# Kernel optimization log

Hardware: AMD Instinct MI355X
Metric: run time of the kernel (lower is better)

The kernel has to match this reference:

```python
import jax, jax.numpy as jnp
import numpy as np

B, S, C, H = 1, 512, 384, 12
SQK, SV, PQK, PV = 16, 16, 4, 8
SCALAR_SCALE = SQK ** -0.5
NEG = jnp.float32(-10000.0)


def _random_rotations(key, shape):
    # Gram-Schmidt on random normals -> proper rotation matrices (rows orthonormal)
    m = jax.random.normal(key, shape + (3, 3), jnp.float32)
    e0 = m[..., 0, :]
    e0 = e0 / jnp.linalg.norm(e0, axis=-1, keepdims=True)
    e1 = m[..., 1, :] - jnp.sum(e0 * m[..., 1, :], axis=-1, keepdims=True) * e0
    e1 = e1 / jnp.linalg.norm(e1, axis=-1, keepdims=True)
    e2 = jnp.cross(e0, e1)
    return jnp.stack([e0, e1, e2], axis=-2)  # [..., 3, 3]


def setup_inputs() -> dict:
    key = jax.random.key(0)
    ks = jax.random.split(key, 24)
    rn = lambda k, shp, s=1.0: jax.random.normal(k, shp, jnp.float32) * s
    w = 0.02  # weight init scale
    inp = {
        'single_repr': rn(ks[0], (B, S, C)),
        'rotations': _random_rotations(ks[1], (B, S)),
        'translations': rn(ks[2], (B, S, 3), 10.0),
        'Wq_s': rn(ks[3], (C, H * SQK), w), 'bq_s': rn(ks[4], (H * SQK,), w),
        'Wk_s': rn(ks[5], (C, H * SQK), w), 'bk_s': rn(ks[6], (H * SQK,), w),
        'Wv_s': rn(ks[7], (C, H * SV), w), 'bv_s': rn(ks[8], (H * SV,), w),
        'Wq_p': rn(ks[9], (C, H * PQK * 3), w), 'bq_p': rn(ks[10], (H * PQK * 3,), w),
        'Wk_p': rn(ks[11], (C, H * PQK * 3), w), 'bk_p': rn(ks[12], (H * PQK * 3,), w),
        'Wv_p': rn(ks[13], (C, H * PV * 3), w), 'bv_p': rn(ks[14], (H * PV * 3,), w),
        'point_weights': rn(ks[15], (H, PQK), 0.5),
        'Wo': rn(ks[16], (H * (SV + PV * 4), C), w), 'bo': rn(ks[17], (C,), w),
        'valid_mask': jax.random.randint(ks[18], (B, S), 0, 2).astype(bool),
    }
    return inp


def _ipa(single_repr, rotations, translations,
         Wq_s, bq_s, Wk_s, bk_s, Wv_s, bv_s,
         Wq_p, bq_p, Wk_p, bk_p, Wv_p, bv_p,
         point_weights, Wo, bo, valid_mask):
    b, s, _ = single_repr.shape
    qs = (single_repr @ Wq_s + bq_s).reshape(b, s, H, SQK)
    ks = (single_repr @ Wk_s + bk_s).reshape(b, s, H, SQK)
    vs = (single_repr @ Wv_s + bv_s).reshape(b, s, H, SV)
    qp = (single_repr @ Wq_p + bq_p).reshape(b, s, H, PQK, 3)
    kp = (single_repr @ Wk_p + bk_p).reshape(b, s, H, PQK, 3)
    vp = (single_repr @ Wv_p + bv_p).reshape(b, s, H, PV, 3)
    t = translations[:, :, None, None, :]
    # local -> global: R @ p + t
    qpg = jnp.einsum('bsij,bshpj->bshpi', rotations, qp) + t
    kpg = jnp.einsum('bsij,bshpj->bshpi', rotations, kp) + t
    vpg = jnp.einsum('bsij,bshpj->bshpi', rotations, vp) + t
    scalar_logits = jnp.einsum('bihd,bjhd->bhij', qs, ks) * SCALAR_SCALE
    # pairwise point distances: [b, i, j, h, p]
    delta = qpg[:, :, None] - kpg[:, None]  # [b, i, j, h, p, 3]
    dist2 = jnp.sum(delta * delta, axis=-1)
    sp_w = jax.nn.softplus(point_weights)  # [H, PQK]
    point_logits = -0.5 * jnp.einsum('bijhp,hp->bhij', dist2, sp_w)
    logits = scalar_logits + point_logits
    key_mask = valid_mask[:, None, None, :]
    logits = jnp.where(key_mask, logits, NEG)
    attn = jax.nn.softmax(logits, axis=-1)
    attn = attn * valid_mask[:, None, :, None].astype(attn.dtype)
    scalar_out = jnp.einsum('bhij,bjhd->bihd', attn, vs).reshape(b, s, H * SV)
    pog = jnp.einsum('bhij,bjhpd->bihpd', attn, vpg)  # [b, s, H, PV, 3]
    # global -> local: R^T (x - t)
    pol = jnp.einsum('bsji,bshpj->bshpi', rotations, pog - t)
    point_norm = jnp.sqrt(jnp.sum(pol * pol, axis=-1))  # [b, s, H, PV]
    combined = jnp.concatenate([
        scalar_out,
        pol.reshape(b, s, H * PV * 3),
        point_norm.reshape(b, s, H * PV),
    ], axis=-1)
    update = combined @ Wo + bo
    return update * valid_mask[..., None].astype(update.dtype)


def reference(single_repr, rotations, translations,
              Wq_s, bq_s, Wk_s, bk_s, Wv_s, bv_s,
              Wq_p, bq_p, Wk_p, bk_p, Wv_p, bv_p,
              point_weights, Wo, bo, valid_mask):
    return _ipa(single_repr, rotations, translations,
                Wq_s, bq_s, Wk_s, bk_s, Wv_s, bv_s,
                Wq_p, bq_p, Wk_p, bk_p, Wv_p, bv_p,
                point_weights, Wo, bo, valid_mask)
```

## Files before the change

kernel.cpp:

```cpp
#include <hip/hip_runtime.h>
#include <math.h>

#define S 512
#define C 384
#define H 12
#define SCALAR_SCALE 0.25f
#define NEG_LOGIT (-10000.0f)

#define XCOLS 1152
#define DQK 28
#define DV 40

__global__ __launch_bounds__(256)
void wcat_kernel(const float* __restrict__ Wq_s, const float* __restrict__ bq_s,
                 const float* __restrict__ Wk_s, const float* __restrict__ bk_s,
                 const float* __restrict__ Wv_s, const float* __restrict__ bv_s,
                 const float* __restrict__ Wq_p, const float* __restrict__ bq_p,
                 const float* __restrict__ Wk_p, const float* __restrict__ bk_p,
                 const float* __restrict__ Wv_p, const float* __restrict__ bv_p,
                 float* __restrict__ Wcat, float* __restrict__ bcat)
{
    const int NW4 = 384 * (XCOLS / 4);
    int t = blockIdx.x * 256 + threadIdx.x;
    if (t < NW4) {
        int k = t / (XCOLS / 4);
        int col = (t - k * (XCOLS / 4)) * 4;
        const float* src;
        if      (col < 192) src = Wq_s + k * 192 + col;
        else if (col < 384) src = Wk_s + k * 192 + (col - 192);
        else if (col < 576) src = Wv_s + k * 192 + (col - 384);
        else if (col < 720) src = Wq_p + k * 144 + (col - 576);
        else if (col < 864) src = Wk_p + k * 144 + (col - 720);
        else                src = Wv_p + k * 288 + (col - 864);
        ((float4*)Wcat)[t] = *(const float4*)src;
    } else if (t < NW4 + XCOLS / 4) {
        int col = (t - NW4) * 4;
        const float* src;
        if      (col < 192) src = bq_s + col;
        else if (col < 384) src = bk_s + (col - 192);
        else if (col < 576) src = bv_s + (col - 384);
        else if (col < 720) src = bq_p + (col - 576);
        else if (col < 864) src = bk_p + (col - 720);
        else                src = bv_p + (col - 864);
        ((float4*)bcat)[t - NW4] = *(const float4*)src;
    }
}

__global__ __launch_bounds__(256)
void gemm64(const float* __restrict__ A, int lda,
            const float* __restrict__ B, int ldb,
            const float* __restrict__ bias,
            float* __restrict__ Cc, int ldc, int K)
{
    __shared__ float As[16][65];
    __shared__ float Bs[16][65];
    const int tid = threadIdx.x;
    const int m0 = blockIdx.y * 64;
    const int n0 = blockIdx.x * 64;
    const int ty = tid >> 4;
    const int tx = tid & 15;

    float acc[4][4] = {};

    for (int k0 = 0; k0 < K; k0 += 16) {
        {
            int r = tid >> 2;
            int c = (tid & 3) * 4;
            const float4 v = *(const float4*)(A + (size_t)(m0 + r) * lda + k0 + c);
            As[c + 0][r] = v.x; As[c + 1][r] = v.y;
            As[c + 2][r] = v.z; As[c + 3][r] = v.w;
        }
        {
            int r = tid >> 4;
            int c = (tid & 15) * 4;
            const float4 v = *(const float4*)(B + (size_t)(k0 + r) * ldb + n0 + c);
            Bs[r][c + 0] = v.x; Bs[r][c + 1] = v.y;
            Bs[r][c + 2] = v.z; Bs[r][c + 3] = v.w;
        }
        __syncthreads();
        #pragma unroll
        for (int k = 0; k < 16; ++k) {
            float a[4], b[4];
            #pragma unroll
            for (int i = 0; i < 4; ++i) a[i] = As[k][ty * 4 + i];
            #pragma unroll
            for (int j = 0; j < 4; ++j) b[j] = Bs[k][tx * 4 + j];
            #pragma unroll
            for (int i = 0; i < 4; ++i)
                #pragma unroll
                for (int j = 0; j < 4; ++j)
                    acc[i][j] += a[i] * b[j];
        }
        __syncthreads();
    }

    #pragma unroll
    for (int i = 0; i < 4; ++i) {
        int m = m0 + ty * 4 + i;
        #pragma unroll
        for (int j = 0; j < 4; ++j) {
            int n = n0 + tx * 4 + j;
            Cc[(size_t)m * ldc + n] = acc[i][j] + bias[n];
        }
    }
}

__global__ __launch_bounds__(256)
void gemm_out(const float* __restrict__ A, int lda,
              const float* __restrict__ B, int ldb,
              const float* __restrict__ bias,
              float* __restrict__ Cc, int ldc, int K,
              const int* __restrict__ rowMask)
{
    __shared__ float As[16][33];
    __shared__ float Bs[16][33];
    const int tid = threadIdx.x;
    const int m0 = blockIdx.y * 32;
    const int n0 = blockIdx.x * 32;
    const int ty = tid >> 4;
    const int tx = tid & 15;

    float acc[2][2] = {};

    for (int k0 = 0; k0 < K; k0 += 16) {
        {
            int r = tid >> 3;
            int c = (tid & 7) * 2;
            const float2 v = *(const float2*)(A + (size_t)(m0 + r) * lda + k0 + c);
            As[c + 0][r] = v.x; As[c + 1][r] = v.y;
        }
        {
            int r = tid >> 4;
            int c = (tid & 15) * 2;
            const float2 v = *(const float2*)(B + (size_t)(k0 + r) * ldb + n0 + c);
            Bs[r][c + 0] = v.x; Bs[r][c + 1] = v.y;
        }
        __syncthreads();
        #pragma unroll
        for (int k = 0; k < 16; ++k) {
            float a0 = As[k][ty * 2], a1 = As[k][ty * 2 + 1];
            float b0 = Bs[k][tx * 2], b1 = Bs[k][tx * 2 + 1];
            acc[0][0] += a0 * b0; acc[0][1] += a0 * b1;
            acc[1][0] += a1 * b0; acc[1][1] += a1 * b1;
        }
        __syncthreads();
    }

    #pragma unroll
    for (int i = 0; i < 2; ++i) {
        int m = m0 + ty * 2 + i;
        float msk = rowMask[m] ? 1.0f : 0.0f;
        #pragma unroll
        for (int j = 0; j < 2; ++j) {
            int n = n0 + tx * 2 + j;
            Cc[(size_t)m * ldc + n] = (acc[i][j] + bias[n]) * msk;
        }
    }
}

__global__ __launch_bounds__(256)
void ipa_points(const float* __restrict__ X,
                const float* __restrict__ rot,
                const float* __restrict__ trans,
                const float* __restrict__ pw,
                float4* __restrict__ Q4, float4* __restrict__ K4,
                float4* __restrict__ V4, float* __restrict__ kb)
{
    int idx = blockIdx.x * 256 + threadIdx.x;
    int h = idx >> 9;
    int s = idx & 511;

    float R[9], t[3];
    #pragma unroll
    for (int i = 0; i < 9; ++i) R[i] = rot[s * 9 + i];
    #pragma unroll
    for (int i = 0; i < 3; ++i) t[i] = trans[s * 3 + i];

    float spw[4];
    #pragma unroll
    for (int p = 0; p < 4; ++p)
        spw[p] = log1pf(__expf(pw[h * 4 + p]));

    const float4* xr4 = (const float4*)(X + (size_t)s * XCOLS);

    float qv[DQK], kv[DQK], vv[DV];
    #pragma unroll
    for (int g = 0; g < 4; ++g) {
        float4 a = xr4[h * 4 + g];
        qv[g * 4 + 0] = a.x * SCALAR_SCALE; qv[g * 4 + 1] = a.y * SCALAR_SCALE;
        qv[g * 4 + 2] = a.z * SCALAR_SCALE; qv[g * 4 + 3] = a.w * SCALAR_SCALE;
        float4 b = xr4[48 + h * 4 + g];
        kv[g * 4 + 0] = b.x; kv[g * 4 + 1] = b.y; kv[g * 4 + 2] = b.z; kv[g * 4 + 3] = b.w;
        float4 c = xr4[96 + h * 4 + g];
        vv[g * 4 + 0] = c.x; vv[g * 4 + 1] = c.y; vv[g * 4 + 2] = c.z; vv[g * 4 + 3] = c.w;
    }
    float qp[12], kp[12], vp[24];
    #pragma unroll
    for (int g = 0; g < 3; ++g) {
        float4 a = xr4[144 + h * 3 + g];
        qp[g * 4 + 0] = a.x; qp[g * 4 + 1] = a.y; qp[g * 4 + 2] = a.z; qp[g * 4 + 3] = a.w;
        float4 b = xr4[180 + h * 3 + g];
        kp[g * 4 + 0] = b.x; kp[g * 4 + 1] = b.y; kp[g * 4 + 2] = b.z; kp[g * 4 + 3] = b.w;
    }
    #pragma unroll
    for (int g = 0; g < 6; ++g) {
        float4 a = xr4[216 + h * 6 + g];
        vp[g * 4 + 0] = a.x; vp[g * 4 + 1] = a.y; vp[g * 4 + 2] = a.z; vp[g * 4 + 3] = a.w;
    }

    float knorm = 0.0f;
    #pragma unroll
    for (int p = 0; p < 4; ++p) {
        #pragma unroll
        for (int i = 0; i < 3; ++i) {
            float qg = R[i * 3] * qp[p * 3] + R[i * 3 + 1] * qp[p * 3 + 1] + R[i * 3 + 2] * qp[p * 3 + 2] + t[i];
            float kg = R[i * 3] * kp[p * 3] + R[i * 3 + 1] * kp[p * 3 + 1] + R[i * 3 + 2] * kp[p * 3 + 2] + t[i];
            qv[16 + p * 3 + i] = spw[p] * qg;
            kv[16 + p * 3 + i] = kg;
            knorm += spw[p] * kg * kg;
        }
    }
    kb[(size_t)h * S + s] = -0.5f * knorm;

    #pragma unroll
    for (int p = 0; p < 8; ++p) {
        #pragma unroll
        for (int i = 0; i < 3; ++i)
            vv[16 + p * 3 + i] = R[i * 3] * vp[p * 3] + R[i * 3 + 1] * vp[p * 3 + 1] + R[i * 3 + 2] * vp[p * 3 + 2] + t[i];
    }

    #pragma unroll
    for (int g = 0; g < 7; ++g)
        Q4[((size_t)h * 7 + g) * S + s] = make_float4(qv[g * 4], qv[g * 4 + 1], qv[g * 4 + 2], qv[g * 4 + 3]);
    #pragma unroll
    for (int g = 0; g < 7; ++g)
        K4[((size_t)h * 7 + g) * S + s] = make_float4(kv[g * 4], kv[g * 4 + 1], kv[g * 4 + 2], kv[g * 4 + 3]);
    #pragma unroll
    for (int g = 0; g < 10; ++g)
        V4[((size_t)h * 10 + g) * S + s] = make_float4(vv[g * 4], vv[g * 4 + 1], vv[g * 4 + 2], vv[g * 4 + 3]);
}

__global__ __launch_bounds__(256)
void ipa_attn(const float4* __restrict__ Q4, const float4* __restrict__ K4,
              const float4* __restrict__ V4, const float* __restrict__ kb,
              const int* __restrict__ valid,
              const float* __restrict__ rot, const float* __restrict__ trans,
              float* __restrict__ combined)
{
    __shared__ float4 sh[4][10];
    const int h = blockIdx.x;
    const int wave = threadIdx.x >> 6;
    const int lane = threadIdx.x & 63;
    const int i = blockIdx.y * 4 + wave;

    float q[DQK];
    #pragma unroll
    for (int g = 0; g < 7; ++g) {
        float4 v = Q4[((size_t)h * 7 + g) * S + i];
        q[g * 4] = v.x; q[g * 4 + 1] = v.y; q[g * 4 + 2] = v.z; q[g * 4 + 3] = v.w;
    }

    const float* kbh = kb + (size_t)h * S;

    float logit[8];
    float mx = -3.0e38f;
    #pragma unroll
    for (int t = 0; t < 8; ++t) {
        int j = t * 64 + lane;
        float dot = kbh[j];
        #pragma unroll
        for (int g = 0; g < 7; ++g) {
            float4 k = K4[((size_t)h * 7 + g) * S + j];
            dot += q[g * 4] * k.x + q[g * 4 + 1] * k.y + q[g * 4 + 2] * k.z + q[g * 4 + 3] * k.w;
        }
        logit[t] = valid[j] ? dot : NEG_LOGIT;
        mx = fmaxf(mx, logit[t]);
    }
    #pragma unroll
    for (int off = 32; off >= 1; off >>= 1)
        mx = fmaxf(mx, __shfl_xor(mx, off, 64));

    float sum = 0.0f;
    #pragma unroll
    for (int t = 0; t < 8; ++t) {
        logit[t] = __expf(logit[t] - mx);
        sum += logit[t];
    }
    #pragma unroll
    for (int off = 32; off >= 1; off >>= 1)
        sum += __shfl_xor(sum, off, 64);
    const float inv = 1.0f / sum;

    float4 acc[10];
    #pragma unroll
    for (int g = 0; g < 10; ++g) acc[g] = make_float4(0.f, 0.f, 0.f, 0.f);
    #pragma unroll
    for (int t = 0; t < 8; ++t) {
        int j = t * 64 + lane;
        float p = logit[t];
        #pragma unroll
        for (int g = 0; g < 10; ++g) {
            float4 v = V4[((size_t)h * 10 + g) * S + j];
            acc[g].x += p * v.x; acc[g].y += p * v.y;
            acc[g].z += p * v.z; acc[g].w += p * v.w;
        }
    }
    #pragma unroll
    for (int g = 0; g < 10; ++g) {
        #pragma unroll
        for (int off = 32; off >= 1; off >>= 1) {
            acc[g].x += __shfl_xor(acc[g].x, off, 64);
            acc[g].y += __shfl_xor(acc[g].y, off, 64);
            acc[g].z += __shfl_xor(acc[g].z, off, 64);
            acc[g].w += __shfl_xor(acc[g].w, off, 64);
        }
    }

    if (lane == 0) {
        #pragma unroll
        for (int g = 0; g < 10; ++g) sh[wave][g] = acc[g];
    }
    const float* shf = (const float*)sh[wave];

    float* crow = combined + (size_t)i * 576;
    if (lane < 16)
        crow[h * 16 + lane] = shf[lane] * inv;

    if (lane < 8) {
        float R[9], t_[3];
        #pragma unroll
        for (int a = 0; a < 9; ++a) R[a] = rot[i * 9 + a];
        #pragma unroll
        for (int a = 0; a < 3; ++a) t_[a] = trans[i * 3 + a];
        int p = lane;
        float d0 = shf[16 + p * 3 + 0] * inv - t_[0];
        float d1 = shf[16 + p * 3 + 1] * inv - t_[1];
        float d2 = shf[16 + p * 3 + 2] * inv - t_[2];
        float pol0 = R[0] * d0 + R[3] * d1 + R[6] * d2;
        float pol1 = R[1] * d0 + R[4] * d1 + R[7] * d2;
        float pol2 = R[2] * d0 + R[5] * d1 + R[8] * d2;
        crow[192 + h * 24 + p * 3 + 0] = pol0;
        crow[192 + h * 24 + p * 3 + 1] = pol1;
        crow[192 + h * 24 + p * 3 + 2] = pol2;
        crow[480 + h * 8 + p] = sqrtf(pol0 * pol0 + pol1 * pol1 + pol2 * pol2);
    }
}

extern "C" void kernel_launch(void* const* d_in, const int* in_sizes, int n_in,
                              void* d_out, int out_size, void* d_ws, size_t ws_size,
                              hipStream_t stream)
{
    const float* single = (const float*)d_in[0];
    const float* rot    = (const float*)d_in[1];
    const float* trans  = (const float*)d_in[2];
    const float* Wq_s   = (const float*)d_in[3];
    const float* bq_s   = (const float*)d_in[4];
    const float* Wk_s   = (const float*)d_in[5];
    const float* bk_s   = (const float*)d_in[6];
    const float* Wv_s   = (const float*)d_in[7];
    const float* bv_s   = (const float*)d_in[8];
    const float* Wq_p   = (const float*)d_in[9];
    const float* bq_p   = (const float*)d_in[10];
    const float* Wk_p   = (const float*)d_in[11];
    const float* bk_p   = (const float*)d_in[12];
    const float* Wv_p   = (const float*)d_in[13];
    const float* bv_p   = (const float*)d_in[14];
    const float* pw     = (const float*)d_in[15];
    const float* Wo     = (const float*)d_in[16];
    const float* bo     = (const float*)d_in[17];
    const int*   valid  = (const int*)d_in[18];

    float* ws = (float*)d_ws;
    float* Wcat     = ws;
    float* bcat     = Wcat + (size_t)384 * XCOLS;
    float* X        = bcat + XCOLS;
    float* Q4f      = X + (size_t)S * XCOLS;
    float* K4f      = Q4f + (size_t)H * 7 * S * 4;
    float* V4f      = K4f + (size_t)H * 7 * S * 4;
    float* kbb      = V4f + (size_t)H * 10 * S * 4;
    float* combined = kbb + (size_t)H * S;

    dim3 blk(256);

    wcat_kernel<<<dim3((384 * (XCOLS / 4) + XCOLS / 4 + 255) / 256), blk, 0, stream>>>(
        Wq_s, bq_s, Wk_s, bk_s, Wv_s, bv_s, Wq_p, bq_p, Wk_p, bk_p, Wv_p, bv_p, Wcat, bcat);

    gemm64<<<dim3(XCOLS / 64, S / 64), blk, 0, stream>>>(single, C, Wcat, XCOLS, bcat, X, XCOLS, C);

    ipa_points<<<dim3(S * H / 256), blk, 0, stream>>>(X, rot, trans, pw,
                                                      (float4*)Q4f, (float4*)K4f, (float4*)V4f, kbb);

    ipa_attn<<<dim3(H, S / 4), blk, 0, stream>>>((const float4*)Q4f, (const float4*)K4f,
                                                 (const float4*)V4f, kbb, valid, rot, trans, combined);

    gemm_out<<<dim3(C / 32, S / 32), blk, 0, stream>>>(combined, 576, Wo, C, bo, (float*)d_out, C, 576, valid);
}
```

Before: 192.5 us.

## Fuse weight concat into projection GEMM and stage K/V tiles in LDS with online softmax

Drops the separate weight/bias concatenation kernel: the projection GEMM now chooses its source weight matrix per thread column and writes float4 outputs with the bias added. The attention kernel now double-buffers each 64-key chunk of K and V in shared memory, shared by the four query waves of a block, and uses an online softmax with a running max and rescaling. This is meant to cut redundant global K/V reads and one launch. In exchange it adds two barriers per chunk, an extra exp per step and more LDS use per block.

```diff
diff --git a/kernel.cpp b/kernel.cpp
--- a/kernel.cpp
+++ b/kernel.cpp
@@ -12,45 +12,14 @@
 #define DV 40
 
 __global__ __launch_bounds__(256)
-void wcat_kernel(const float* __restrict__ Wq_s, const float* __restrict__ bq_s,
-                 const float* __restrict__ Wk_s, const float* __restrict__ bk_s,
-                 const float* __restrict__ Wv_s, const float* __restrict__ bv_s,
-                 const float* __restrict__ Wq_p, const float* __restrict__ bq_p,
-                 const float* __restrict__ Wk_p, const float* __restrict__ bk_p,
-                 const float* __restrict__ Wv_p, const float* __restrict__ bv_p,
-                 float* __restrict__ Wcat, float* __restrict__ bcat)
-{
-    const int NW4 = 384 * (XCOLS / 4);
-    int t = blockIdx.x * 256 + threadIdx.x;
-    if (t < NW4) {
-        int k = t / (XCOLS / 4);
-        int col = (t - k * (XCOLS / 4)) * 4;
-        const float* src;
-        if      (col < 192) src = Wq_s + k * 192 + col;
-        else if (col < 384) src = Wk_s + k * 192 + (col - 192);
-        else if (col < 576) src = Wv_s + k * 192 + (col - 384);
-        else if (col < 720) src = Wq_p + k * 144 + (col - 576);
-        else if (col < 864) src = Wk_p + k * 144 + (col - 720);
-        else                src = Wv_p + k * 288 + (col - 864);
-        ((float4*)Wcat)[t] = *(const float4*)src;
-    } else if (t < NW4 + XCOLS / 4) {
-        int col = (t - NW4) * 4;
-        const float* src;
-        if      (col < 192) src = bq_s + col;
-        else if (col < 384) src = bk_s + (col - 192);
-        else if (col < 576) src = bv_s + (col - 384);
-        else if (col < 720) src = bq_p + (col - 576);
-        else if (col < 864) src = bk_p + (col - 720);
-        else                src = bv_p + (col - 864);
-        ((float4*)bcat)[t - NW4] = *(const float4*)src;
-    }
-}
-
-__global__ __launch_bounds__(256)
-void gemm64(const float* __restrict__ A, int lda,
-            const float* __restrict__ B, int ldb,
-            const float* __restrict__ bias,
-            float* __restrict__ Cc, int ldc, int K)
+void gemm_proj(const float* __restrict__ A,
+               const float* __restrict__ Wq_s, const float* __restrict__ bq_s,
+               const float* __restrict__ Wk_s, const float* __restrict__ bk_s,
+               const float* __restrict__ Wv_s, const float* __restrict__ bv_s,
+               const float* __restrict__ Wq_p, const float* __restrict__ bq_p,
+               const float* __restrict__ Wk_p, const float* __restrict__ bk_p,
+               const float* __restrict__ Wv_p, const float* __restrict__ bv_p,
+               float* __restrict__ X)
 {
     __shared__ float As[16][65];
     __shared__ float Bs[16][65];
@@ -60,20 +29,29 @@
     const int ty = tid >> 4;
     const int tx = tid & 15;
 
+    const int n = n0 + tx * 4;
+    const float* bsrc; const float* bbias; int ldbs, ncol;
+    if      (n < 192) { bsrc = Wq_s; bbias = bq_s; ldbs = 192; ncol = n; }
+    else if (n < 384) { bsrc = Wk_s; bbias = bk_s; ldbs = 192; ncol = n - 192; }
+    else if (n < 576) { bsrc = Wv_s; bbias = bv_s; ldbs = 192; ncol = n - 384; }
+    else if (n < 720) { bsrc = Wq_p; bbias = bq_p; ldbs = 144; ncol = n - 576; }
+    else if (n < 864) { bsrc = Wk_p; bbias = bk_p; ldbs = 144; ncol = n - 720; }
+    else              { bsrc = Wv_p; bbias = bv_p; ldbs = 288; ncol = n - 864; }
+
     float acc[4][4] = {};
 
-    for (int k0 = 0; k0 < K; k0 += 16) {
+    for (int k0 = 0; k0 < C; k0 += 16) {
         {
             int r = tid >> 2;
             int c = (tid & 3) * 4;
-            const float4 v = *(const float4*)(A + (size_t)(m0 + r) * lda + k0 + c);
+            const float4 v = *(const float4*)(A + (size_t)(m0 + r) * C + k0 + c);
             As[c + 0][r] = v.x; As[c + 1][r] = v.y;
             As[c + 2][r] = v.z; As[c + 3][r] = v.w;
         }
         {
             int r = tid >> 4;
-            int c = (tid & 15) * 4;
-            const float4 v = *(const float4*)(B + (size_t)(k0 + r) * ldb + n0 + c);
+            const float4 v = *(const float4*)(bsrc + (size_t)(k0 + r) * ldbs + ncol);
+            int c = tx * 4;
             Bs[r][c + 0] = v.x; Bs[r][c + 1] = v.y;
             Bs[r][c + 2] = v.z; Bs[r][c + 3] = v.w;
         }
@@ -94,14 +72,13 @@
         __syncthreads();
     }
 
+    const float4 bb = *(const float4*)(bbias + ncol);
     #pragma unroll
     for (int i = 0; i < 4; ++i) {
         int m = m0 + ty * 4 + i;
-        #pragma unroll
-        for (int j = 0; j < 4; ++j) {
-            int n = n0 + tx * 4 + j;
-            Cc[(size_t)m * ldc + n] = acc[i][j] + bias[n];
-        }
+        float4 o = make_float4(acc[i][0] + bb.x, acc[i][1] + bb.y,
+                               acc[i][2] + bb.z, acc[i][3] + bb.w);
+        *(float4*)(X + (size_t)m * XCOLS + n) = o;
     }
 }
 
@@ -247,10 +224,13 @@
               const float* __restrict__ rot, const float* __restrict__ trans,
               float* __restrict__ combined)
 {
+    __shared__ float4 Kl[2][448];
+    __shared__ float4 Vl[2][640];
     __shared__ float4 sh[4][10];
     const int h = blockIdx.x;
-    const int wave = threadIdx.x >> 6;
-    const int lane = threadIdx.x & 63;
+    const int tid = threadIdx.x;
+    const int wave = tid >> 6;
+    const int lane = tid & 63;
     const int i = blockIdx.y * 4 + wave;
 
     float q[DQK];
@@ -259,52 +239,80 @@
         float4 v = Q4[((size_t)h * 7 + g) * S + i];
         q[g * 4] = v.x; q[g * 4 + 1] = v.y; q[g * 4 + 2] = v.z; q[g * 4 + 3] = v.w;
     }
-
-    const float* kbh = kb + (size_t)h * S;
-
-    float logit[8];
-    float mx = -3.0e38f;
+    float kbv[8]; int vld[8];
     #pragma unroll
     for (int t = 0; t < 8; ++t) {
-        int j = t * 64 + lane;
-        float dot = kbh[j];
+        kbv[t] = kb[(size_t)h * S + t * 64 + lane];
+        vld[t] = valid[t * 64 + lane];
+    }
+
+    Kl[0][tid] = K4[((size_t)h * 7 + (tid >> 6)) * S + (tid & 63)];
+    if (tid < 192)
+        Kl[0][tid + 256] = K4[((size_t)h * 7 + ((tid + 256) >> 6)) * S + ((tid + 256) & 63)];
+    Vl[0][tid] = V4[((size_t)h * 10 + (tid >> 6)) * S + (tid & 63)];
+    Vl[0][tid + 256] = V4[((size_t)h * 10 + ((tid + 256) >> 6)) * S + ((tid + 256) & 63)];
+    if (tid < 128)
+        Vl[0][tid + 512] = V4[((size_t)h * 10 + ((tid + 512) >> 6)) * S + ((tid + 512) & 63)];
+
+    float4 acc[10];
+    #pragma unroll
+    for (int g = 0; g < 10; ++g) acc[g] = make_float4(0.f, 0.f, 0.f, 0.f);
+    float m = -3.0e38f, sum = 0.0f;
+    float4 rk0, rk1, rv0, rv1, rv2;
+
+    #pragma unroll
+    for (int t = 0; t < 8; ++t) {
+        const int b = t & 1, nb = b ^ 1;
+        if (t < 7) {
+            const int t0 = (t + 1) * 64;
+            rk0 = K4[((size_t)h * 7 + (tid >> 6)) * S + t0 + (tid & 63)];
+            if (tid < 192)
+                rk1 = K4[((size_t)h * 7 + ((tid + 256) >> 6)) * S + t0 + ((tid + 256) & 63)];
+            rv0 = V4[((size_t)h * 10 + (tid >> 6)) * S + t0 + (tid & 63)];
+            rv1 = V4[((size_t)h * 10 + ((tid + 256) >> 6)) * S + t0 + ((tid + 256) & 63)];
+            if (tid < 128)
+                rv2 = V4[((size_t)h * 10 + ((tid + 512) >> 6)) * S + t0 + ((tid + 512) & 63)];
+        }
+        __syncthreads();
+
+        float dot = kbv[t];
         #pragma unroll
         for (int g = 0; g < 7; ++g) {
-            float4 k = K4[((size_t)h * 7 + g) * S + j];
+            float4 k = Kl[b][g * 64 + lane];
             dot += q[g * 4] * k.x + q[g * 4 + 1] * k.y + q[g * 4 + 2] * k.z + q[g * 4 + 3] * k.w;
         }
-        logit[t] = valid[j] ? dot : NEG_LOGIT;
-        mx = fmaxf(mx, logit[t]);
-    }
-    #pragma unroll
-    for (int off = 32; off >= 1; off >>= 1)
-        mx = fmaxf(mx, __shfl_xor(mx, off, 64));
-
-    float sum = 0.0f;
-    #pragma unroll
-    for (int t = 0; t < 8; ++t) {
-        logit[t] = __expf(logit[t] - mx);
-        sum += logit[t];
-    }
+        float lg = vld[t] ? dot : NEG_LOGIT;
+        float lm = lg;
+        #pragma unroll
+        for (int off = 32; off >= 1; off >>= 1)
+            lm = fmaxf(lm, __shfl_xor(lm, off, 64));
+        float mnew = fmaxf(m, lm);
+        float sc = __expf(m - mnew);
+        float p = __expf(lg - mnew);
+        sum = sum * sc + p;
+        #pragma unroll
+        for (int g = 0; g < 10; ++g) {
+            float4 v = Vl[b][g * 64 + lane];
+            acc[g].x = acc[g].x * sc + p * v.x;
+            acc[g].y = acc[g].y * sc + p * v.y;
+            acc[g].z = acc[g].z * sc + p * v.z;
+            acc[g].w = acc[g].w * sc + p * v.w;
+        }
+        m = mnew;
+
+        __syncthreads();
+        if (t < 7) {
+            Kl[nb][tid] = rk0;
+            if (tid < 192) Kl[nb][tid + 256] = rk1;
+            Vl[nb][tid] = rv0;
+            Vl[nb][tid + 256] = rv1;
+            if (tid < 128) Vl[nb][tid + 512] = rv2;
+        }
+    }
+
     #pragma unroll
     for (int off = 32; off >= 1; off >>= 1)
         sum += __shfl_xor(sum, off, 64);
-    const float inv = 1.0f / sum;
-
-    float4 acc[10];
-    #pragma unroll
-    for (int g = 0; g < 10; ++g) acc[g] = make_float4(0.f, 0.f, 0.f, 0.f);
-    #pragma unroll
-    for (int t = 0; t < 8; ++t) {
-        int j = t * 64 + lane;
-        float p = logit[t];
-        #pragma unroll
-        for (int g = 0; g < 10; ++g) {
-            float4 v = V4[((size_t)h * 10 + g) * S + j];
-            acc[g].x += p * v.x; acc[g].y += p * v.y;
-            acc[g].z += p * v.z; acc[g].w += p * v.w;
-        }
-    }
     #pragma unroll
     for (int g = 0; g < 10; ++g) {
         #pragma unroll
@@ -315,6 +323,7 @@
             acc[g].w += __shfl_xor(acc[g].w, off, 64);
         }
     }
+    const float inv = 1.0f / sum;
 
     if (lane == 0) {
         #pragma unroll
@@ -371,9 +380,7 @@
     const int*   valid  = (const int*)d_in[18];
 
     float* ws = (float*)d_ws;
-    float* Wcat     = ws;
-    float* bcat     = Wcat + (size_t)384 * XCOLS;
-    float* X        = bcat + XCOLS;
+    float* X        = ws;
     float* Q4f      = X + (size_t)S * XCOLS;
     float* K4f      = Q4f + (size_t)H * 7 * S * 4;
     float* V4f      = K4f + (size_t)H * 7 * S * 4;
@@ -382,10 +389,9 @@
 
     dim3 blk(256);
 
-    wcat_kernel<<<dim3((384 * (XCOLS / 4) + XCOLS / 4 + 255) / 256), blk, 0, stream>>>(
-        Wq_s, bq_s, Wk_s, bk_s, Wv_s, bv_s, Wq_p, bq_p, Wk_p, bk_p, Wv_p, bv_p, Wcat, bcat);
-
-    gemm64<<<dim3(XCOLS / 64, S / 64), blk, 0, stream>>>(single, C, Wcat, XCOLS, bcat, X, XCOLS, C);
+    gemm_proj<<<dim3(XCOLS / 64, S / 64), blk, 0, stream>>>(
+        single, Wq_s, bq_s, Wk_s, bk_s, Wv_s, bv_s,
+        Wq_p, bq_p, Wk_p, bk_p, Wv_p, bv_p, X);
 
     ipa_points<<<dim3(S * H / 256), blk, 0, stream>>>(X, rot, trans, pw,
                                                       (float4*)Q4f, (float4*)K4f, (float4*)V4f, kbb);
```

Measured after the change: 225.3 us. 17.0% more time.

## Fuse weight concatenation into projection GEMM and widen K tiles

Applied to the files above, without the earlier changes.

Drops the separate kernel that copied the six projection weight matrices into a concatenated buffer. The projection GEMM now picks the source matrix and bias per column group and reads them directly, saving one launch and a pass over about 1.7 MB of weights. Both GEMMs also take larger K steps (48 and 32) with float4 loads and stores, so there are fewer barrier iterations. The cost is more shared memory per block, which may lower occupancy.

```diff
diff --git a/kernel.cpp b/kernel.cpp
--- a/kernel.cpp
+++ b/kernel.cpp
@@ -12,74 +12,59 @@
 #define DV 40
 
 __global__ __launch_bounds__(256)
-void wcat_kernel(const float* __restrict__ Wq_s, const float* __restrict__ bq_s,
-                 const float* __restrict__ Wk_s, const float* __restrict__ bk_s,
-                 const float* __restrict__ Wv_s, const float* __restrict__ bv_s,
-                 const float* __restrict__ Wq_p, const float* __restrict__ bq_p,
-                 const float* __restrict__ Wk_p, const float* __restrict__ bk_p,
-                 const float* __restrict__ Wv_p, const float* __restrict__ bv_p,
-                 float* __restrict__ Wcat, float* __restrict__ bcat)
-{
-    const int NW4 = 384 * (XCOLS / 4);
-    int t = blockIdx.x * 256 + threadIdx.x;
-    if (t < NW4) {
-        int k = t / (XCOLS / 4);
-        int col = (t - k * (XCOLS / 4)) * 4;
-        const float* src;
-        if      (col < 192) src = Wq_s + k * 192 + col;
-        else if (col < 384) src = Wk_s + k * 192 + (col - 192);
-        else if (col < 576) src = Wv_s + k * 192 + (col - 384);
-        else if (col < 720) src = Wq_p + k * 144 + (col - 576);
-        else if (col < 864) src = Wk_p + k * 144 + (col - 720);
-        else                src = Wv_p + k * 288 + (col - 864);
-        ((float4*)Wcat)[t] = *(const float4*)src;
-    } else if (t < NW4 + XCOLS / 4) {
-        int col = (t - NW4) * 4;
-        const float* src;
-        if      (col < 192) src = bq_s + col;
-        else if (col < 384) src = bk_s + (col - 192);
-        else if (col < 576) src = bv_s + (col - 384);
-        else if (col < 720) src = bq_p + (col - 576);
-        else if (col < 864) src = bk_p + (col - 720);
-        else                src = bv_p + (col - 864);
-        ((float4*)bcat)[t - NW4] = *(const float4*)src;
-    }
-}
-
-__global__ __launch_bounds__(256)
-void gemm64(const float* __restrict__ A, int lda,
-            const float* __restrict__ B, int ldb,
-            const float* __restrict__ bias,
-            float* __restrict__ Cc, int ldc, int K)
-{
-    __shared__ float As[16][65];
-    __shared__ float Bs[16][65];
+void gemm_proj(const float* __restrict__ A,
+               const float* __restrict__ Wq_s, const float* __restrict__ bq_s,
+               const float* __restrict__ Wk_s, const float* __restrict__ bk_s,
+               const float* __restrict__ Wv_s, const float* __restrict__ bv_s,
+               const float* __restrict__ Wq_p, const float* __restrict__ bq_p,
+               const float* __restrict__ Wk_p, const float* __restrict__ bk_p,
+               const float* __restrict__ Wv_p, const float* __restrict__ bv_p,
+               float* __restrict__ X)
+{
+    __shared__ float As[48][65];
+    __shared__ float Bs[48][65];
     const int tid = threadIdx.x;
     const int m0 = blockIdx.y * 64;
     const int n0 = blockIdx.x * 64;
     const int ty = tid >> 4;
     const int tx = tid & 15;
 
+    const int n = n0 + tx * 4;
+    const float* bsrc; const float* bbias; int ldbs, ncol;
+    if      (n < 192) { bsrc = Wq_s; bbias = bq_s; ldbs = 192; ncol = n; }
+    else if (n < 384) { bsrc = Wk_s; bbias = bk_s; ldbs = 192; ncol = n - 192; }
+    else if (n < 576) { bsrc = Wv_s; bbias = bv_s; ldbs = 192; ncol = n - 384; }
+    else if (n < 720) { bsrc = Wq_p; bbias = bq_p; ldbs = 144; ncol = n - 576; }
+    else if (n < 864) { bsrc = Wk_p; bbias = bk_p; ldbs = 144; ncol = n - 720; }
+    else              { bsrc = Wv_p; bbias = bv_p; ldbs = 288; ncol = n - 864; }
+
     float acc[4][4] = {};
 
-    for (int k0 = 0; k0 < K; k0 += 16) {
+    for (int k0 = 0; k0 < C; k0 += 48) {
         {
             int r = tid >> 2;
-            int c = (tid & 3) * 4;
-            const float4 v = *(const float4*)(A + (size_t)(m0 + r) * lda + k0 + c);
-            As[c + 0][r] = v.x; As[c + 1][r] = v.y;
-            As[c + 2][r] = v.z; As[c + 3][r] = v.w;
+            int cbase = (tid & 3) * 4;
+            #pragma unroll
+            for (int cc = 0; cc < 3; ++cc) {
+                int c = cbase + cc * 16;
+                const float4 v = *(const float4*)(A + (size_t)(m0 + r) * C + k0 + c);
+                As[c + 0][r] = v.x; As[c + 1][r] = v.y;
+                As[c + 2][r] = v.z; As[c + 3][r] = v.w;
+            }
         }
         {
             int r = tid >> 4;
-            int c = (tid & 15) * 4;
-            const float4 v = *(const float4*)(B + (size_t)(k0 + r) * ldb + n0 + c);
-            Bs[r][c + 0] = v.x; Bs[r][c + 1] = v.y;
-            Bs[r][c + 2] = v.z; Bs[r][c + 3] = v.w;
+            int c = tx * 4;
+            #pragma unroll
+            for (int rr = 0; rr < 3; ++rr) {
+                const float4 v = *(const float4*)(bsrc + (size_t)(k0 + r + rr * 16) * ldbs + ncol);
+                Bs[r + rr * 16][c + 0] = v.x; Bs[r + rr * 16][c + 1] = v.y;
+                Bs[r + rr * 16][c + 2] = v.z; Bs[r + rr * 16][c + 3] = v.w;
+            }
         }
         __syncthreads();
         #pragma unroll
-        for (int k = 0; k < 16; ++k) {
+        for (int k = 0; k < 48; ++k) {
             float a[4], b[4];
             #pragma unroll
             for (int i = 0; i < 4; ++i) a[i] = As[k][ty * 4 + i];
@@ -94,14 +79,13 @@
         __syncthreads();
     }
 
+    const float4 bb = *(const float4*)(bbias + ncol);
     #pragma unroll
     for (int i = 0; i < 4; ++i) {
         int m = m0 + ty * 4 + i;
-        #pragma unroll
-        for (int j = 0; j < 4; ++j) {
-            int n = n0 + tx * 4 + j;
-            Cc[(size_t)m * ldc + n] = acc[i][j] + bias[n];
-        }
+        float4 o = make_float4(acc[i][0] + bb.x, acc[i][1] + bb.y,
+                               acc[i][2] + bb.z, acc[i][3] + bb.w);
+        *(float4*)(X + (size_t)m * XCOLS + n) = o;
     }
 }
 
@@ -112,8 +96,8 @@
               float* __restrict__ Cc, int ldc, int K,
               const int* __restrict__ rowMask)
 {
-    __shared__ float As[16][33];
-    __shared__ float Bs[16][33];
+    __shared__ float As[32][33];
+    __shared__ float Bs[32][33];
     const int tid = threadIdx.x;
     const int m0 = blockIdx.y * 32;
     const int n0 = blockIdx.x * 32;
@@ -122,22 +106,24 @@
 
     float acc[2][2] = {};
 
-    for (int k0 = 0; k0 < K; k0 += 16) {
+    for (int k0 = 0; k0 < K; k0 += 32) {
         {
             int r = tid >> 3;
-            int c = (tid & 7) * 2;
-            const float2 v = *(const float2*)(A + (size_t)(m0 + r) * lda + k0 + c);
+            int c = (tid & 7) * 4;
+            const float4 v = *(const float4*)(A + (size_t)(m0 + r) * lda + k0 + c);
             As[c + 0][r] = v.x; As[c + 1][r] = v.y;
+            As[c + 2][r] = v.z; As[c + 3][r] = v.w;
         }
         {
-            int r = tid >> 4;
-            int c = (tid & 15) * 2;
-            const float2 v = *(const float2*)(B + (size_t)(k0 + r) * ldb + n0 + c);
+            int r = tid >> 3;
+            int c = (tid & 7) * 4;
+            const float4 v = *(const float4*)(B + (size_t)(k0 + r) * ldb + n0 + c);
             Bs[r][c + 0] = v.x; Bs[r][c + 1] = v.y;
+            Bs[r][c + 2] = v.z; Bs[r][c + 3] = v.w;
         }
         __syncthreads();
         #pragma unroll
-        for (int k = 0; k < 16; ++k) {
+        for (int k = 0; k < 32; ++k) {
             float a0 = As[k][ty * 2], a1 = As[k][ty * 2 + 1];
             float b0 = Bs[k][tx * 2], b1 = Bs[k][tx * 2 + 1];
             acc[0][0] += a0 * b0; acc[0][1] += a0 * b1;
@@ -371,9 +357,7 @@
     const int*   valid  = (const int*)d_in[18];
 
     float* ws = (float*)d_ws;
-    float* Wcat     = ws;
-    float* bcat     = Wcat + (size_t)384 * XCOLS;
-    float* X        = bcat + XCOLS;
+    float* X        = ws;
     float* Q4f      = X + (size_t)S * XCOLS;
     float* K4f      = Q4f + (size_t)H * 7 * S * 4;
     float* V4f      = K4f + (size_t)H * 7 * S * 4;
@@ -382,10 +366,9 @@
 
     dim3 blk(256);
 
-    wcat_kernel<<<dim3((384 * (XCOLS / 4) + XCOLS / 4 + 255) / 256), blk, 0, stream>>>(
-        Wq_s, bq_s, Wk_s, bk_s, Wv_s, bv_s, Wq_p, bq_p, Wk_p, bk_p, Wv_p, bv_p, Wcat, bcat);
-
-    gemm64<<<dim3(XCOLS / 64, S / 64), blk, 0, stream>>>(single, C, Wcat, XCOLS, bcat, X, XCOLS, C);
+    gemm_proj<<<dim3(XCOLS / 64, S / 64), blk, 0, stream>>>(
+        single, Wq_s, bq_s, Wk_s, bk_s, Wv_s, bv_s,
+        Wq_p, bq_p, Wk_p, bk_p, Wv_p, bv_p, X);
 
     ipa_points<<<dim3(S * H / 256), blk, 0, stream>>>(X, rot, trans, pw,
                                                       (float4*)Q4f, (float4*)K4f, (float4*)V4f, kbb);
```

After: 189.3 us. Within noise of the previous version (-1.7%).
